# Performance work log

Hardware: AMD Instinct MI355X
Metric: run time of the kernel (lower is better)

Reference implementation:

```python
import jax, jax.numpy as jnp
import numpy as np

B, S, H, E = 8, 2048, 1024, 8

def setup_inputs() -> dict:
    key = jax.random.key(0)
    ks = jax.random.split(key, 7)
    sc = 1.0 / np.sqrt(H)
    return {
        "x":   jax.random.normal(ks[0], (B, S, H), dtype=jnp.float32),
        "We":  jax.random.normal(ks[1], (E, H, H), dtype=jnp.float32) * sc,
        "be":  jax.random.normal(ks[2], (E, H), dtype=jnp.float32) * 0.01,
        "Wr1": jax.random.normal(ks[3], (H, H), dtype=jnp.float32) * sc,
        "br1": jax.random.normal(ks[4], (H,), dtype=jnp.float32) * 0.01,
        "Wr2": jax.random.normal(ks[5], (H, E), dtype=jnp.float32) * sc,
        "br2": jax.random.normal(ks[6], (E,), dtype=jnp.float32) * 0.01,
    }

def reference(x, We, be, Wr1, br1, Wr2, br2):
    # Router: mean over seq -> Linear+ReLU -> Linear -> softmax over experts
    x_mean = x.mean(axis=1)                                   # [B,H]
    h = jax.nn.relu(x_mean @ Wr1 + br1)                        # [B,H]
    routing = jax.nn.softmax(h @ Wr2 + br2, axis=-1)           # [B,E]
    # Dense all-experts MLP: every expert processes every token
    eo = jax.nn.relu(jnp.einsum('bsh,ehd->ebsd', x, We)
                     + be[:, None, None, :])                   # [E,B,S,H]
    # KV caches are zero-initialized and read before any update in the
    # original forward, so their additive contribution is zero here.
    out = jnp.einsum('ebsd,be->bsd', eo, routing)              # [B,S,H]
    return out
```

## Files before the change

kernel.cpp:

```cpp
#include <hip/hip_runtime.h>
#include <stdint.h>

#define Hdim 1024
#define Bdim 8
#define Sdim 2048
#define Edim 8
#define Mtot 16384
#define Ntot 8192

typedef short bf16x8 __attribute__((ext_vector_type(8)));
typedef unsigned short u16x8 __attribute__((ext_vector_type(8)));
typedef float f32x4 __attribute__((ext_vector_type(4)));

__device__ __forceinline__ unsigned short f2bf(float f) {
  union { float f; unsigned u; } v; v.f = f;
  unsigned r = (v.u + 0x7FFFu + ((v.u >> 16) & 1u)) >> 16;
  return (unsigned short)r;
}

__device__ __forceinline__ void gload16(const void* g, void* l) {
  __builtin_amdgcn_global_load_lds((const __attribute__((address_space(1))) void*)g,
                                   (__attribute__((address_space(3))) void*)l,
                                   16, 0, 0);
}

#define VMCNT_(N) asm volatile("s_waitcnt vmcnt(" #N ")" ::: "memory")
#define VMCNT(N) VMCNT_(N)
#define BAR() __builtin_amdgcn_s_barrier()

__global__ void k_convert_mean(const float* __restrict__ x,
                               unsigned short* __restrict__ xb,
                               float* __restrict__ part) {
  const int b = blockIdx.y;
  const int s0 = blockIdx.x * 32;
  const int t = threadIdx.x;
  const int hg = (t & 127) << 3;
  const int sp = t >> 7;
  float accv[8];
#pragma unroll
  for (int q = 0; q < 8; ++q) accv[q] = 0.f;
#pragma unroll 4
  for (int i = 0; i < 16; ++i) {
    const int s = s0 + sp + (i << 1);
    const size_t base = ((size_t)b * Sdim + s) * Hdim + hg;
    const float4 lo = *(const float4*)(x + base);
    const float4 hi = *(const float4*)(x + base + 4);
    accv[0] += lo.x; accv[1] += lo.y; accv[2] += lo.z; accv[3] += lo.w;
    accv[4] += hi.x; accv[5] += hi.y; accv[6] += hi.z; accv[7] += hi.w;
    u16x8 pk;
    pk[0] = f2bf(lo.x); pk[1] = f2bf(lo.y); pk[2] = f2bf(lo.z); pk[3] = f2bf(lo.w);
    pk[4] = f2bf(hi.x); pk[5] = f2bf(hi.y); pk[6] = f2bf(hi.z); pk[7] = f2bf(hi.w);
    *(u16x8*)(xb + base) = pk;
  }
  float* pp = part + ((size_t)b * 128 + blockIdx.x * 2 + sp) * Hdim + hg;
#pragma unroll
  for (int q = 0; q < 8; ++q) pp[q] = accv[q];
}

__global__ void k_transpose_w(const float* __restrict__ We,
                              unsigned short* __restrict__ wt) {
  __shared__ float lds[64][65];
  const int e = blockIdx.z, hb = blockIdx.y, db = blockIdx.x;
  const int t = threadIdx.x;
  const float* src = We + ((size_t)e * Hdim + hb * 64) * Hdim + db * 64;
#pragma unroll 4
  for (int it = 0; it < 16; ++it) {
    int idx = it * 256 + t;
    int r = idx >> 6, c = idx & 63;
    lds[r][c] = src[(size_t)r * Hdim + c];
  }
  __syncthreads();
#pragma unroll 4
  for (int it = 0; it < 16; ++it) {
    int idx = it * 256 + t;
    int r = idx >> 6, c = idx & 63;
    const int np = (db * 64 + r) * 8 + e;
    wt[(size_t)np * Hdim + hb * 64 + c] = f2bf(lds[c][r]);
  }
}

__global__ void k_mean(const float* __restrict__ part, float* __restrict__ xm) {
  __shared__ float red[4][64];
  const int b = blockIdx.y, hc = blockIdx.x, t = threadIdx.x;
  const int h = hc * 64 + (t & 63), q = t >> 6;
  float s = 0.f;
  const float* p = part + ((size_t)b * 128 + q * 32) * Hdim + h;
#pragma unroll 8
  for (int c = 0; c < 32; ++c) s += p[(size_t)c * Hdim];
  red[q][t & 63] = s;
  __syncthreads();
  if (t < 64) {
    float v = (red[0][t] + red[1][t]) + (red[2][t] + red[3][t]);
    xm[b * Hdim + hc * 64 + t] = v * (1.0f / 2048.0f);
  }
}

__global__ void k_r1(const float* __restrict__ xm,
                     const float* __restrict__ Wr1,
                     const float* __restrict__ br1,
                     float* __restrict__ hbuf) {
  __shared__ float xs[Hdim];
  __shared__ float hred[2][128];
  const int b = blockIdx.y, jc = blockIdx.x, t = threadIdx.x;
  for (int k = t; k < Hdim; k += 256) xs[k] = xm[b * Hdim + k];
  __syncthreads();
  const int j = jc * 128 + (t & 127);
  const int kh = (t >> 7) * 512;
  float acc = 0.f;
#pragma unroll 8
  for (int k = 0; k < 512; ++k)
    acc = fmaf(xs[kh + k], Wr1[(size_t)(kh + k) * Hdim + j], acc);
  hred[t >> 7][t & 127] = acc;
  __syncthreads();
  if (t < 128)
    hbuf[b * Hdim + jc * 128 + t] =
        fmaxf(hred[0][t] + hred[1][t] + br1[jc * 128 + t], 0.f);
}

__global__ void k_router2(const float* __restrict__ hbuf,
                          const float* __restrict__ Wr2,
                          const float* __restrict__ br2,
                          float* __restrict__ routing) {
  const int t = threadIdx.x;
  const int e = t & 7;
  const int b = t >> 3;
  float acc = br2[e];
  const float* hb = hbuf + b * Hdim;
#pragma unroll 8
  for (int k = 0; k < Hdim; ++k) acc = fmaf(hb[k], Wr2[k * Edim + e], acc);
  float m = acc;
  for (int d = 1; d < 8; d <<= 1) m = fmaxf(m, __shfl_xor(m, d, 64));
  float p = __expf(acc - m);
  float s = p;
  for (int d = 1; d < 8; d <<= 1) s += __shfl_xor(s, d, 64);
  routing[t] = p / s;
}

__global__ __launch_bounds__(512, 2)
void k_moe_gemm(const unsigned short* __restrict__ xb,
                const unsigned short* __restrict__ wt,
                const float* __restrict__ be,
                const float* __restrict__ routing,
                float* __restrict__ out) {
  extern __shared__ char smem[];
  const int t = threadIdx.x;
  const int wave = t >> 6, lane = t & 63;
  const int la15 = lane & 15;
  const int wr = wave >> 2;
  const int wcn = wave & 3;

  const int bid = blockIdx.x;
  const int xcd = bid & 7;
  const int idx = bid >> 3;
  const int rnd = idx >> 5;
  const int slot = idx & 31;
  const int m0 = (xcd * 8 + (slot & 7)) * 256;
  const int n0 = (rnd * 4 + (slot >> 3)) * 256;

  const int cx = (((lane & 7) ^ (lane >> 3)) << 3);
  const unsigned short* aStage = xb + (size_t)(m0 + wave * 8 + (lane >> 3)) * Hdim + cx;
  const int bRowLoc = ((wave & 3) << 3) + ((wave >> 2) << 6) + (lane >> 3);
  const unsigned short* bStage = wt + (size_t)(n0 + bRowLoc) * Hdim + cx;
  const int aLdsW = wave * 1024;
  const int bLdsW = ((wave & 3) << 10) + ((wave >> 2) << 13);

  const int swz0 = (((lane >> 4) ^ (lane & 7)) << 4);
  const int swz1 = ((((lane >> 4) + 4) ^ (lane & 7)) << 4);
  const int aRd = (wr * 128 + la15) * 128;
  const int bRd = (wcn * 64 + la15) * 128;

  f32x4 acc[8][4];
#pragma unroll
  for (int i = 0; i < 8; ++i)
#pragma unroll
    for (int j = 0; j < 4; ++j) acc[i][j] = (f32x4){0.f, 0.f, 0.f, 0.f};

  bf16x8 a0[4][2], a1[4][2], b0[2][2], b1[2][2];

#define STG_A(half, buf, k0) do { \
    gload16(aStage + (half) * 64 * 1024 + (k0),          smem + (buf) * 32768 + aLdsW + (half) * 8192); \
    gload16(aStage + (128 + (half) * 64) * 1024 + (k0),  smem + (buf) * 32768 + aLdsW + 16384 + (half) * 8192); \
  } while (0)
#define STG_B(sub, buf, k0) do { \
    gload16(bStage + (sub) * 32 * 1024 + (k0),           smem + 65536 + (buf) * 32768 + bLdsW + (sub) * 4096); \
    gload16(bStage + (128 + (sub) * 32) * 1024 + (k0),   smem + 65536 + (buf) * 32768 + bLdsW + 16384 + (sub) * 4096); \
  } while (0)
#define LD_A(dst, buf, qi) do { \
    _Pragma("unroll") for (int ii = 0; ii < 4; ++ii) { \
      dst[ii][0] = *(const bf16x8*)(smem + (buf) * 32768 + aRd + (qi) * 8192 + ii * 2048 + swz0); \
      dst[ii][1] = *(const bf16x8*)(smem + (buf) * 32768 + aRd + (qi) * 8192 + ii * 2048 + swz1); } \
  } while (0)
#define LD_A_LO(dst, buf, qi) do { \
    _Pragma("unroll") for (int ii = 0; ii < 2; ++ii) { \
      dst[ii][0] = *(const bf16x8*)(smem + (buf) * 32768 + aRd + (qi) * 8192 + ii * 2048 + swz0); \
      dst[ii][1] = *(const bf16x8*)(smem + (buf) * 32768 + aRd + (qi) * 8192 + ii * 2048 + swz1); } \
  } while (0)
#define LD_A_HI(dst, buf, qi) do { \
    _Pragma("unroll") for (int ii = 2; ii < 4; ++ii) { \
      dst[ii][0] = *(const bf16x8*)(smem + (buf) * 32768 + aRd + (qi) * 8192 + ii * 2048 + swz0); \
      dst[ii][1] = *(const bf16x8*)(smem + (buf) * 32768 + aRd + (qi) * 8192 + ii * 2048 + swz1); } \
  } while (0)
#define LD_B(dst, buf, qj) do { \
    _Pragma("unroll") for (int jj = 0; jj < 2; ++jj) { \
      dst[jj][0] = *(const bf16x8*)(smem + 65536 + (buf) * 32768 + bRd + (qj) * 4096 + jj * 2048 + swz0); \
      dst[jj][1] = *(const bf16x8*)(smem + 65536 + (buf) * 32768 + bRd + (qj) * 4096 + jj * 2048 + swz1); } \
  } while (0)
#define MF_Q(af_, bf_, qi, jh) do { \
    __builtin_amdgcn_s_setprio(1); \
    _Pragma("unroll") for (int ii = 0; ii < 4; ++ii) \
      _Pragma("unroll") for (int jj = 0; jj < 2; ++jj) { \
        acc[(qi)*4+ii][(jh)*2+jj] = __builtin_amdgcn_mfma_f32_16x16x32_bf16(af_[ii][0], bf_[jj][0], acc[(qi)*4+ii][(jh)*2+jj], 0, 0, 0); \
        acc[(qi)*4+ii][(jh)*2+jj] = __builtin_amdgcn_mfma_f32_16x16x32_bf16(af_[ii][1], bf_[jj][1], acc[(qi)*4+ii][(jh)*2+jj], 0, 0, 0); } \
    __builtin_amdgcn_s_setprio(0); \
  } while (0)

  STG_A(0, 0, 0);
  STG_B(0, 0, 0);
  STG_B(1, 0, 0);
  STG_A(1, 0, 0);
  STG_A(0, 1, 64);
  STG_B(0, 1, 64);
  STG_B(1, 1, 64);
  STG_A(1, 1, 64);
  VMCNT(4);
  BAR();
  LD_A(a0, 0, 0);
  LD_B(b1, 0, 1);

#pragma unroll 1
  for (int j = 0; j < 8; ++j) {
    const int k2 = (j * 128 + 128) & 1023;
    const int k3 = (j * 128 + 192) & 1023;
    LD_B(b0, 0, 0);
    LD_A_LO(a1, 0, 1);
    STG_A(0, 0, k2);
    BAR();
    MF_Q(a0, b0, 0, 0);
    BAR();
    LD_A_HI(a1, 0, 1);
    STG_B(0, 0, k2);
    VMCNT(4);
    BAR();
    MF_Q(a0, b1, 0, 1);
    BAR();
    LD_A(a0, 1, 0);
    STG_B(1, 0, k2);
    BAR();
    MF_Q(a1, b1, 1, 1);
    BAR();
    LD_B(b1, 1, 1);
    STG_A(1, 0, k2);
    BAR();
    MF_Q(a1, b0, 1, 0);
    BAR();
    LD_B(b0, 1, 0);
    LD_A_LO(a1, 1, 1);
    STG_A(0, 1, k3);
    BAR();
    MF_Q(a0, b0, 0, 0);
    BAR();
    LD_A_HI(a1, 1, 1);
    STG_B(0, 1, k3);
    VMCNT(4);
    BAR();
    MF_Q(a0, b1, 0, 1);
    BAR();
    LD_A(a0, 0, 0);
    STG_B(1, 1, k3);
    BAR();
    MF_Q(a1, b1, 1, 1);
    BAR();
    LD_B(b1, 0, 1);
    STG_A(1, 1, k3);
    BAR();
    MF_Q(a1, b0, 1, 0);
    BAR();
  }

  VMCNT(0);
  BAR();

  float* outb = (float*)smem;
  const int bidx = m0 >> 11;
  const float rw = routing[bidx * Edim + (lane & 7)];
  const int dblk = (lane >> 3) & 1;
  const bool writer = ((lane & 7) == 0);
#pragma unroll
  for (int j = 0; j < 4; ++j) {
    const int col0 = wcn * 64 + j * 16;
    const float bias = be[(lane & 7) * Hdim + (n0 >> 3) + (col0 >> 3) + dblk];
#pragma unroll
    for (int i = 0; i < 8; ++i) {
#pragma unroll
      for (int r = 0; r < 4; ++r) {
        float v = fmaxf(acc[i][j][r] + bias, 0.f) * rw;
        v += __shfl_xor(v, 1, 64);
        v += __shfl_xor(v, 2, 64);
        v += __shfl_xor(v, 4, 64);
        if (writer) {
          const int row = wr * 128 + i * 16 + ((lane >> 4) << 2) + r;
          outb[row * 33 + (col0 >> 3) + dblk] = v;
        }
      }
    }
  }
  BAR();
  const size_t obase = (size_t)m0 * Hdim + (n0 >> 3);
#pragma unroll
  for (int it = 0; it < 4; ++it) {
    const int r = it * 64 + (t >> 3);
    const int c = (t & 7) * 4;
    float4 vv;
    vv.x = outb[r * 33 + c];
    vv.y = outb[r * 33 + c + 1];
    vv.z = outb[r * 33 + c + 2];
    vv.w = outb[r * 33 + c + 3];
    *(float4*)(out + obase + (size_t)r * Hdim + c) = vv;
  }
#undef STG_A
#undef STG_B
#undef LD_A
#undef LD_A_LO
#undef LD_A_HI
#undef LD_B
#undef MF_Q
}

extern "C" void kernel_launch(void* const* d_in, const int* in_sizes, int n_in,
                              void* d_out, int out_size, void* d_ws, size_t ws_size,
                              hipStream_t stream) {
  const float* x   = (const float*)d_in[0];
  const float* We  = (const float*)d_in[1];
  const float* be  = (const float*)d_in[2];
  const float* Wr1 = (const float*)d_in[3];
  const float* br1 = (const float*)d_in[4];
  const float* Wr2 = (const float*)d_in[5];
  const float* br2 = (const float*)d_in[6];
  float* out = (float*)d_out;

  char* ws = (char*)d_ws;
  unsigned short* xb = (unsigned short*)ws;
  unsigned short* wt = (unsigned short*)(ws + 33554432);
  float* part    = (float*)(ws + 50331648);
  float* xm      = (float*)(ws + 54525952);
  float* hbuf    = (float*)(ws + 54558720);
  float* routing = (float*)(ws + 54591488);

  hipFuncSetAttribute((const void*)k_moe_gemm,
                      hipFuncAttributeMaxDynamicSharedMemorySize, 131072);

  k_convert_mean<<<dim3(Sdim / 32, Bdim), 256, 0, stream>>>(x, xb, part);
  k_transpose_w<<<dim3(Hdim / 64, Hdim / 64, Edim), 256, 0, stream>>>(We, wt);
  k_mean<<<dim3(16, Bdim), 256, 0, stream>>>(part, xm);
  k_r1<<<dim3(8, Bdim), 256, 0, stream>>>(xm, Wr1, br1, hbuf);
  k_router2<<<1, 64, 0, stream>>>(hbuf, Wr2, br2, routing);
  k_moe_gemm<<<dim3(2048), 512, 131072, stream>>>(xb, wt, be, routing, out);
}
```

Measured before the change: 421.5 us.

## Restructure GEMM main loop to one barrier per phase with explicit lgkm waits

Rewrites the double-buffered bf16 MFMA main loop so each phase issues LDS reads and the next global-to-LDS stage, then performs a single vmcnt/barrier/lgkmcnt wait before its MFMA quarter. The old schedule used two barriers per phase. A third B register set is added so B fragments can rotate between even and odd buffers, and sched_barrier pins the instruction order. The prologue now stages only the first buffer and waits for it fully. This is meant to cut barrier stalls and overlap memory with math more tightly, at the cost of more registers and a fragile hand-tuned wait count that could race or spill.

```diff
diff --git a/kernel.cpp b/kernel.cpp
--- a/kernel.cpp
+++ b/kernel.cpp
@@ -26,6 +26,9 @@
 
 #define VMCNT_(N) asm volatile("s_waitcnt vmcnt(" #N ")" ::: "memory")
 #define VMCNT(N) VMCNT_(N)
+#define LGKM_(N) asm volatile("s_waitcnt lgkmcnt(" #N ")" ::: "memory")
+#define LGKM(N) LGKM_(N)
+#define SCHED0() __builtin_amdgcn_sched_barrier(0)
 #define BAR() __builtin_amdgcn_s_barrier()
 
 __global__ void k_convert_mean(const float* __restrict__ x,
@@ -175,7 +178,7 @@
 #pragma unroll
     for (int j = 0; j < 4; ++j) acc[i][j] = (f32x4){0.f, 0.f, 0.f, 0.f};
 
-  bf16x8 a0[4][2], a1[4][2], b0[2][2], b1[2][2];
+  bf16x8 aA[4][2], aB[4][2], bB[2][2], bAe[2][2], bAo[2][2];
 
 #define STG_A(half, buf, k0) do { \
     gload16(aStage + (half) * 64 * 1024 + (k0),          smem + (buf) * 32768 + aLdsW + (half) * 8192); \
@@ -187,16 +190,6 @@
   } while (0)
 #define LD_A(dst, buf, qi) do { \
     _Pragma("unroll") for (int ii = 0; ii < 4; ++ii) { \
-      dst[ii][0] = *(const bf16x8*)(smem + (buf) * 32768 + aRd + (qi) * 8192 + ii * 2048 + swz0); \
-      dst[ii][1] = *(const bf16x8*)(smem + (buf) * 32768 + aRd + (qi) * 8192 + ii * 2048 + swz1); } \
-  } while (0)
-#define LD_A_LO(dst, buf, qi) do { \
-    _Pragma("unroll") for (int ii = 0; ii < 2; ++ii) { \
-      dst[ii][0] = *(const bf16x8*)(smem + (buf) * 32768 + aRd + (qi) * 8192 + ii * 2048 + swz0); \
-      dst[ii][1] = *(const bf16x8*)(smem + (buf) * 32768 + aRd + (qi) * 8192 + ii * 2048 + swz1); } \
-  } while (0)
-#define LD_A_HI(dst, buf, qi) do { \
-    _Pragma("unroll") for (int ii = 2; ii < 4; ++ii) { \
       dst[ii][0] = *(const bf16x8*)(smem + (buf) * 32768 + aRd + (qi) * 8192 + ii * 2048 + swz0); \
       dst[ii][1] = *(const bf16x8*)(smem + (buf) * 32768 + aRd + (qi) * 8192 + ii * 2048 + swz1); } \
   } while (0)
@@ -214,67 +207,46 @@
     __builtin_amdgcn_s_setprio(0); \
   } while (0)
 
+#define PH_AFTER(LGN) VMCNT(2); BAR(); LGKM(LGN); SCHED0()
+
   STG_A(0, 0, 0);
   STG_B(0, 0, 0);
   STG_B(1, 0, 0);
   STG_A(1, 0, 0);
-  STG_A(0, 1, 64);
-  STG_B(0, 1, 64);
-  STG_B(1, 1, 64);
-  STG_A(1, 1, 64);
-  VMCNT(4);
+  VMCNT(0);
   BAR();
-  LD_A(a0, 0, 0);
-  LD_B(b1, 0, 1);
+  LD_B(bAe, 0, 0);
+  LD_A(aA, 0, 0);
+  SCHED0();
 
 #pragma unroll 1
   for (int j = 0; j < 8; ++j) {
+    const int k1 = j * 128 + 64;
     const int k2 = (j * 128 + 128) & 1023;
-    const int k3 = (j * 128 + 192) & 1023;
-    LD_B(b0, 0, 0);
-    LD_A_LO(a1, 0, 1);
-    STG_A(0, 0, k2);
-    BAR();
-    MF_Q(a0, b0, 0, 0);
-    BAR();
-    LD_A_HI(a1, 0, 1);
-    STG_B(0, 0, k2);
-    VMCNT(4);
-    BAR();
-    MF_Q(a0, b1, 0, 1);
-    BAR();
-    LD_A(a0, 1, 0);
-    STG_B(1, 0, k2);
-    BAR();
-    MF_Q(a1, b1, 1, 1);
-    BAR();
-    LD_B(b1, 1, 1);
-    STG_A(1, 0, k2);
-    BAR();
-    MF_Q(a1, b0, 1, 0);
-    BAR();
-    LD_B(b0, 1, 0);
-    LD_A_LO(a1, 1, 1);
-    STG_A(0, 1, k3);
-    BAR();
-    MF_Q(a0, b0, 0, 0);
-    BAR();
-    LD_A_HI(a1, 1, 1);
-    STG_B(0, 1, k3);
-    VMCNT(4);
-    BAR();
-    MF_Q(a0, b1, 0, 1);
-    BAR();
-    LD_A(a0, 0, 0);
-    STG_B(1, 1, k3);
-    BAR();
-    MF_Q(a1, b1, 1, 1);
-    BAR();
-    LD_B(b1, 0, 1);
-    STG_A(1, 1, k3);
-    BAR();
-    MF_Q(a1, b0, 1, 0);
-    BAR();
+    LD_B(bB, 0, 1); SCHED0(); STG_B(0, 1, k1);
+    PH_AFTER(4);
+    MF_Q(aA, bAe, 0, 0);
+    LD_A(aB, 0, 1); SCHED0(); STG_A(0, 1, k1);
+    PH_AFTER(8);
+    MF_Q(aA, bB, 0, 1);
+    LD_B(bAo, 1, 0); SCHED0(); STG_B(1, 1, k1);
+    PH_AFTER(4);
+    MF_Q(aB, bB, 1, 1);
+    LD_A(aA, 1, 0); SCHED0(); STG_A(1, 1, k1);
+    PH_AFTER(8);
+    MF_Q(aB, bAe, 1, 0);
+    LD_B(bB, 1, 1); SCHED0(); STG_B(0, 0, k2);
+    PH_AFTER(4);
+    MF_Q(aA, bAo, 0, 0);
+    LD_A(aB, 1, 1); SCHED0(); STG_A(0, 0, k2);
+    PH_AFTER(8);
+    MF_Q(aA, bB, 0, 1);
+    LD_B(bAe, 0, 0); SCHED0(); STG_B(1, 0, k2);
+    PH_AFTER(4);
+    MF_Q(aB, bB, 1, 1);
+    LD_A(aA, 0, 0); SCHED0(); STG_A(1, 0, k2);
+    PH_AFTER(8);
+    MF_Q(aB, bAo, 1, 0);
   }
 
   VMCNT(0);
@@ -320,10 +292,9 @@
 #undef STG_A
 #undef STG_B
 #undef LD_A
-#undef LD_A_LO
-#undef LD_A_HI
 #undef LD_B
 #undef MF_Q
+#undef PH_AFTER
 }
 
 extern "C" void kernel_launch(void* const* d_in, const int* in_sizes, int n_in,
```

Result: slower. 534.8 us (+26.9%).
